# Optimization experiments

Hardware: AMD Instinct MI355X
Metric: run time of the kernel (lower is better)

Reference implementation:

```python
import jax, jax.numpy as jnp
import numpy as np

B, S, D, OUT = 16, 2048, 64, 128

def setup_inputs() -> dict:
    key = jax.random.key(0)
    k1, k2, k3 = jax.random.split(key, 3)
    input_ = jax.random.normal(k1, (B, S, D), dtype=jnp.float32)
    # Linear(sequence_length -> output_features): W [out, S], b [out]
    W = jax.random.normal(k2, (OUT, S), dtype=jnp.float32) * (1.0 / np.sqrt(S))
    b = jax.random.normal(k3, (OUT,), dtype=jnp.float32) * 0.01
    return {"input_": input_, "W": W, "b": b}

def reference(input_, W, b):
    # Per-batch Gram matrix X @ X^T: [B, S, S]
    x_squared = jnp.einsum('bsd,btd->bst', input_, input_)
    # Linear over the last (sequence) dim: [B, S, out]
    out = jnp.einsum('bst,ot->bso', x_squared, W) + b
    return out
```

## Files before the change

### kernel.cpp

```cpp
#include <hip/hip_runtime.h>

#define BB 16
#define SS 2048
#define DD 64
#define OO 128
#define SPL 16
#define YEL (OO * DD)

typedef __attribute__((ext_vector_type(8))) short short8;
typedef __attribute__((ext_vector_type(4))) float f32x4;

__device__ __forceinline__ unsigned short f2bf(float f) {
    unsigned int u = __float_as_uint(f);
    return (unsigned short)((u + 0x7FFF + ((u >> 16) & 1)) >> 16);
}
__device__ __forceinline__ unsigned int pk2(float x, float y) {
    return (unsigned int)f2bf(x) | ((unsigned int)f2bf(y) << 16);
}
__device__ __forceinline__ short8 cvt8(float4 a, float4 b) {
    uint4 u = make_uint4(pk2(a.x, a.y), pk2(a.z, a.w), pk2(b.x, b.y), pk2(b.z, b.w));
    return *(short8*)&u;
}
__device__ __forceinline__ float bflo(unsigned int u) { return __uint_as_float(u << 16); }
__device__ __forceinline__ float bfhi(unsigned int u) { return __uint_as_float(u & 0xffff0000u); }

__device__ __forceinline__ int yswz(int o, int d) {
    return (o << 6) + ((((d >> 3) ^ (o & 7)) << 3) | (d & 7));
}

__global__ __launch_bounds__(512) void k_yf(const float* __restrict__ X,
                                            const float* __restrict__ W,
                                            unsigned short* __restrict__ YpB) {
    __shared__ unsigned short XT[64 * 132];

    const int bx  = blockIdx.x;
    const int b   = bx & 15;
    const int p   = bx >> 4;
    const int t0  = p * (SS / SPL);
    const int tid = threadIdx.x;
    const int w   = tid >> 6;
    const int l   = tid & 63;

    const float* Xb = X + ((size_t)b * SS + t0) * DD;
#pragma unroll
    for (int i = 0; i < 4; ++i) {
        const int tl = w * 4 + i * 32;
        const float x0 = Xb[(size_t)(tl + 0) * DD + l];
        const float x1 = Xb[(size_t)(tl + 1) * DD + l];
        const float x2 = Xb[(size_t)(tl + 2) * DD + l];
        const float x3 = Xb[(size_t)(tl + 3) * DD + l];
        *(uint2*)&XT[l * 132 + tl] = make_uint2(pk2(x0, x1), pk2(x2, x3));
    }
    __syncthreads();

    const int n = l & 15;
    const int q = l >> 4;

    f32x4 acc[4];
#pragma unroll
    for (int j = 0; j < 4; ++j) acc[j] = {0.f, 0.f, 0.f, 0.f};

    const float* Wr = W + (size_t)(w * 16 + n) * SS + t0;
#pragma unroll
    for (int kk = 0; kk < SS / SPL; kk += 32) {
        const float4 wa = *(const float4*)(Wr + kk + q * 8);
        const float4 wb = *(const float4*)(Wr + kk + q * 8 + 4);
        const short8 a  = cvt8(wa, wb);
#pragma unroll
        for (int j = 0; j < 4; ++j) {
            const unsigned short* r = &XT[(j * 16 + n) * 132 + kk + q * 8];
            const uint2 lo = *(const uint2*)(r);
            const uint2 hi = *(const uint2*)(r + 4);
            uint4 u = make_uint4(lo.x, lo.y, hi.x, hi.y);
            acc[j] = __builtin_amdgcn_mfma_f32_16x16x32_bf16(a, *(short8*)&u, acc[j], 0, 0, 0);
        }
    }

    unsigned short* slab = YpB + (size_t)(b * SPL + p) * YEL;
#pragma unroll
    for (int j = 0; j < 4; ++j)
#pragma unroll
        for (int r = 0; r < 4; ++r)
            slab[yswz(w * 16 + q * 4 + r, j * 16 + n)] = f2bf(acc[j][r]);
}

__global__ __launch_bounds__(512) void k_out2(const float* __restrict__ X,
                                              const unsigned short* __restrict__ YpB,
                                              const float* __restrict__ bias,
                                              float* __restrict__ out) {
    __shared__ unsigned short YL[YEL];

    const int bx  = blockIdx.x;
    const int b   = bx & 15;
    const int st  = bx >> 4;
    const int tid = threadIdx.x;
    const int w   = tid >> 6;
    const int l   = tid & 63;
    const int n   = l & 15;
    const int q   = l >> 4;

    const uint4* Yb4 = (const uint4*)(YpB + (size_t)b * SPL * YEL);
#pragma unroll
    for (int c = tid; c < YEL / 8; c += 512) {
        float s[8];
#pragma unroll
        for (int e = 0; e < 8; ++e) s[e] = 0.f;
#pragma unroll
        for (int pp = 0; pp < SPL; ++pp) {
            const uint4 v = Yb4[(size_t)pp * (YEL / 8) + c];
            s[0] += bflo(v.x); s[1] += bfhi(v.x);
            s[2] += bflo(v.y); s[3] += bfhi(v.y);
            s[4] += bflo(v.z); s[5] += bfhi(v.z);
            s[6] += bflo(v.w); s[7] += bfhi(v.w);
        }
        ((uint4*)YL)[c] = make_uint4(pk2(s[0], s[1]), pk2(s[2], s[3]),
                                     pk2(s[4], s[5]), pk2(s[6], s[7]));
    }

    const int s0 = st * 128;
    float bv[8];
#pragma unroll
    for (int j = 0; j < 8; ++j) bv[j] = bias[j * 16 + n];

    f32x4 acc[8];
#pragma unroll
    for (int j = 0; j < 8; ++j) acc[j] = {0.f, 0.f, 0.f, 0.f};

    __syncthreads();

    const float* Xr = X + ((size_t)b * SS + s0 + w * 16 + n) * DD;
#pragma unroll
    for (int kk = 0; kk < DD; kk += 32) {
        const float4 xa = *(const float4*)(Xr + kk + q * 8);
        const float4 xb = *(const float4*)(Xr + kk + q * 8 + 4);
        const short8 a  = cvt8(xa, xb);
        const int c8    = (kk >> 3) + q;
#pragma unroll
        for (int j = 0; j < 8; ++j) {
            const int o = j * 16 + n;
            const uint4 u = *(const uint4*)&YL[(o << 6) + (((c8 ^ (o & 7)) << 3))];
            acc[j] = __builtin_amdgcn_mfma_f32_16x16x32_bf16(a, *(short8*)&u, acc[j], 0, 0, 0);
        }
    }

    float* op = out + ((size_t)b * SS + s0 + w * 16 + q * 4) * OO;
#pragma unroll
    for (int j = 0; j < 8; ++j)
#pragma unroll
        for (int r = 0; r < 4; ++r)
            op[(size_t)r * OO + j * 16 + n] = acc[j][r] + bv[j];
}

extern "C" void kernel_launch(void* const* d_in, const int* in_sizes, int n_in,
                              void* d_out, int out_size, void* d_ws, size_t ws_size,
                              hipStream_t stream) {
    const float* X    = (const float*)d_in[0];
    const float* W    = (const float*)d_in[1];
    const float* bias = (const float*)d_in[2];
    float* out = (float*)d_out;

    unsigned short* YpB = (unsigned short*)d_ws;

    k_yf <<<dim3(256), dim3(512), 0, stream>>>(X, W, YpB);
    k_out2<<<dim3(256), dim3(512), 0, stream>>>(X, YpB, bias, out);
}
```

Measured before the change: 76.65 us.

## Fold split-K partial sums into MFMA accumulation instead of reducing into LDS

The second kernel no longer sums the 16 partial Y slabs into shared memory before the GEMM. It now issues MFMAs directly against each partial slab read from global memory, so the reduction happens inside the MFMA accumulators. This removes the LDS staging, the block barrier and the bf16 re-rounding of the summed Y. The cost is 16x more MFMA work and many more global/L2 reads per block, and the first kernel drops its swizzled layout to match the plain global reads.

```diff
diff --git a/kernel.cpp b/kernel.cpp
--- a/kernel.cpp
+++ b/kernel.cpp
@@ -20,12 +20,6 @@
 __device__ __forceinline__ short8 cvt8(float4 a, float4 b) {
     uint4 u = make_uint4(pk2(a.x, a.y), pk2(a.z, a.w), pk2(b.x, b.y), pk2(b.z, b.w));
     return *(short8*)&u;
-}
-__device__ __forceinline__ float bflo(unsigned int u) { return __uint_as_float(u << 16); }
-__device__ __forceinline__ float bfhi(unsigned int u) { return __uint_as_float(u & 0xffff0000u); }
-
-__device__ __forceinline__ int yswz(int o, int d) {
-    return (o << 6) + ((((d >> 3) ^ (o & 7)) << 3) | (d & 7));
 }
 
 __global__ __launch_bounds__(512) void k_yf(const float* __restrict__ X,
@@ -81,15 +75,13 @@
     for (int j = 0; j < 4; ++j)
 #pragma unroll
         for (int r = 0; r < 4; ++r)
-            slab[yswz(w * 16 + q * 4 + r, j * 16 + n)] = f2bf(acc[j][r]);
+            slab[((w * 16 + q * 4 + r) << 6) + (j * 16 + n)] = f2bf(acc[j][r]);
 }
 
-__global__ __launch_bounds__(512) void k_out2(const float* __restrict__ X,
+__global__ __launch_bounds__(512) void k_out3(const float* __restrict__ X,
                                               const unsigned short* __restrict__ YpB,
                                               const float* __restrict__ bias,
                                               float* __restrict__ out) {
-    __shared__ unsigned short YL[YEL];
-
     const int bx  = blockIdx.x;
     const int b   = bx & 15;
     const int st  = bx >> 4;
@@ -99,25 +91,14 @@
     const int n   = l & 15;
     const int q   = l >> 4;
 
-    const uint4* Yb4 = (const uint4*)(YpB + (size_t)b * SPL * YEL);
+    short8 apre[2];
+    const float* Xr = X + ((size_t)b * SS + st * 128 + w * 16 + n) * DD;
 #pragma unroll
-    for (int c = tid; c < YEL / 8; c += 512) {
-        float s[8];
-#pragma unroll
-        for (int e = 0; e < 8; ++e) s[e] = 0.f;
-#pragma unroll
-        for (int pp = 0; pp < SPL; ++pp) {
-            const uint4 v = Yb4[(size_t)pp * (YEL / 8) + c];
-            s[0] += bflo(v.x); s[1] += bfhi(v.x);
-            s[2] += bflo(v.y); s[3] += bfhi(v.y);
-            s[4] += bflo(v.z); s[5] += bfhi(v.z);
-            s[6] += bflo(v.w); s[7] += bfhi(v.w);
-        }
-        ((uint4*)YL)[c] = make_uint4(pk2(s[0], s[1]), pk2(s[2], s[3]),
-                                     pk2(s[4], s[5]), pk2(s[6], s[7]));
+    for (int kk = 0; kk < DD; kk += 32) {
+        const float4 xa = *(const float4*)(Xr + kk + q * 8);
+        const float4 xb = *(const float4*)(Xr + kk + q * 8 + 4);
+        apre[kk >> 5] = cvt8(xa, xb);
     }
-
-    const int s0 = st * 128;
     float bv[8];
 #pragma unroll
     for (int j = 0; j < 8; ++j) bv[j] = bias[j * 16 + n];
@@ -126,24 +107,24 @@
 #pragma unroll
     for (int j = 0; j < 8; ++j) acc[j] = {0.f, 0.f, 0.f, 0.f};
 
-    __syncthreads();
-
-    const float* Xr = X + ((size_t)b * SS + s0 + w * 16 + n) * DD;
+    const unsigned short* Sb = YpB + (size_t)b * SPL * YEL;
+#pragma unroll 4
+    for (int p = 0; p < SPL; ++p) {
+        const unsigned short* sp = Sb + (size_t)p * YEL;
 #pragma unroll
-    for (int kk = 0; kk < DD; kk += 32) {
-        const float4 xa = *(const float4*)(Xr + kk + q * 8);
-        const float4 xb = *(const float4*)(Xr + kk + q * 8 + 4);
-        const short8 a  = cvt8(xa, xb);
-        const int c8    = (kk >> 3) + q;
+        for (int kk = 0; kk < DD; kk += 32) {
+            const short8 a = apre[kk >> 5];
+            const int d0   = kk + q * 8;
 #pragma unroll
-        for (int j = 0; j < 8; ++j) {
-            const int o = j * 16 + n;
-            const uint4 u = *(const uint4*)&YL[(o << 6) + (((c8 ^ (o & 7)) << 3))];
-            acc[j] = __builtin_amdgcn_mfma_f32_16x16x32_bf16(a, *(short8*)&u, acc[j], 0, 0, 0);
+            for (int j = 0; j < 8; ++j) {
+                const int o = j * 16 + n;
+                const uint4 u = *(const uint4*)&sp[(o << 6) + d0];
+                acc[j] = __builtin_amdgcn_mfma_f32_16x16x32_bf16(a, *(short8*)&u, acc[j], 0, 0, 0);
+            }
         }
     }
 
-    float* op = out + ((size_t)b * SS + s0 + w * 16 + q * 4) * OO;
+    float* op = out + ((size_t)b * SS + st * 128 + w * 16 + q * 4) * OO;
 #pragma unroll
     for (int j = 0; j < 8; ++j)
 #pragma unroll
@@ -161,6 +142,6 @@
 
     unsigned short* YpB = (unsigned short*)d_ws;
 
-    k_yf <<<dim3(256), dim3(512), 0, stream>>>(X, W, YpB);
-    k_out2<<<dim3(256), dim3(512), 0, stream>>>(X, YpB, bias, out);
+    k_yf  <<<dim3(256), dim3(512), 0, stream>>>(X, W, YpB);
+    k_out3<<<dim3(256), dim3(512), 0, stream>>>(X, YpB, bias, out);
 }
```

Result: slower. 129.2 us (+68.6%).
